# Kernel tuning notes

Hardware: AMD Instinct MI355X
Metric: run time of the kernel (lower is better)

The kernel has to match this reference:

```python
import jax, jax.numpy as jnp
import numpy as np

B, S, D = 2, 512, 1024   # batch, seq, hidden_size
E, K, I = 16, 8, 1024    # num_experts, num_experts_per_tok, moe_intermediate_size
I_SH = 1024              # moe_intermediate_size * num_shared_experts
ROUTE_SCALE = 2.826


def setup_inputs() -> dict:
    key = jax.random.key(0)
    ks = jax.random.split(key, 8)
    s = 0.02
    return {
        "x": jax.random.normal(ks[0], (B, S, D), dtype=jnp.float32),
        "gate_w": jax.random.normal(ks[1], (E, D), dtype=jnp.float32) * s,
        "expert_bias": jnp.zeros((E,), dtype=jnp.float32),
        "w_gate": jax.random.normal(ks[2], (E, I, D), dtype=jnp.float32) * s,
        "w_up": jax.random.normal(ks[3], (E, I, D), dtype=jnp.float32) * s,
        "w_down": jax.random.normal(ks[4], (E, D, I), dtype=jnp.float32) * s,
        "shared_gate_w": jax.random.normal(ks[5], (I_SH, D), dtype=jnp.float32) * s,
        "shared_up_w": jax.random.normal(ks[6], (I_SH, D), dtype=jnp.float32) * s,
        "shared_down_w": jax.random.normal(ks[7], (D, I_SH), dtype=jnp.float32) * s,
    }


def reference(x, gate_w, expert_bias, w_gate, w_up, w_down,
              shared_gate_w, shared_up_w, shared_down_w):
    # --- routing (sigmoid scores, top-k, optional norm, scale) ---
    gates = jnp.einsum('bsd,ed->bse', x, gate_w)
    scores = jax.nn.sigmoid(gates.astype(jnp.float32))           # [B,S,E]
    sel_scores = scores + expert_bias
    _, inds = jax.lax.top_k(sel_scores, K)                       # [B,S,K]
    selected = jnp.take_along_axis(scores, inds, axis=-1)        # [B,S,K]
    selected = selected / selected.sum(axis=-1, keepdims=True)   # route_norm (K>1)
    selected = selected * ROUTE_SCALE
    # combine weights as dense [B,S,E]; unselected experts get weight 0,
    # which is mathematically identical to gather-dispatch-combine.
    onehot = jax.nn.one_hot(inds, E, dtype=selected.dtype)       # [B,S,K,E]
    combine = jnp.einsum('bske,bsk->bse', onehot, selected)
    # --- experts (SwitchGLU: per-expert SwiGLU MLPs) ---
    hg = jnp.einsum('bsd,eid->bsei', x, w_gate)                  # [B,S,E,I]
    hu = jnp.einsum('bsd,eid->bsei', x, w_up)
    h = jax.nn.silu(hg) * hu
    ye = jnp.einsum('bsei,edi->bsed', h, w_down)                 # [B,S,E,D]
    y = jnp.einsum('bsed,bse->bsd', ye, combine).astype(x.dtype)
    # --- shared expert MLP (SwiGLU) ---
    g = jnp.einsum('bsd,id->bsi', x, shared_gate_w)
    u = jnp.einsum('bsd,id->bsi', x, shared_up_w)
    y = y + jnp.einsum('bsi,di->bsd', jax.nn.silu(g) * u, shared_down_w)
    return y
```

## Files before the change

kernel.cpp:

```cpp
#include <hip/hip_runtime.h>
#include <hip/hip_bf16.h>


typedef __attribute__((ext_vector_type(8))) short bf16x8;
typedef __attribute__((ext_vector_type(4))) float f32x4;
typedef __attribute__((ext_vector_type(8))) unsigned short u16x8;

#define NTOK 1024
#define DD   1024
#define II   1024
#define NE   16
#define NEXP 17
#define KSEL 8
#define RSCALE 2.826f

#define WCONV_BLOCKS 2176
#define ROUTE_BLOCKS 256

#define BM 128
#define BN 64
#define BK 32
#define LDA 40

#define MB (1024ull*1024ull)
#define OFF_XBF   0ull
#define OFF_H     (2ull*MB)
#define OFF_WG    (36ull*MB)
#define OFF_WU    (70ull*MB)
#define OFF_WD    (104ull*MB)
#define OFF_LIST  (138ull*MB)
#define OFF_SCALE (OFF_LIST + 4ull*NEXP*NTOK)
#define OFF_CNT   (OFF_SCALE + 4ull*NEXP*NTOK)
#define WS_NEED   (OFF_CNT + 4096ull)
#define OFF_POS   WS_NEED
#define OFF_PBUF  (OFF_POS + 4ull*NE*NTOK)
#define WS_NEED2  (OFF_PBUF + 4ull*9216*DD)

__device__ __forceinline__ unsigned short f2bf(float f) {
    union { __hip_bfloat16 h; unsigned short u; } c;
    c.h = __float2bfloat16(f);
    return c.u;
}

__device__ __forceinline__ void gl2lds16(const unsigned short* g, unsigned short* l) {
    __builtin_amdgcn_global_load_lds(
        (const __attribute__((address_space(1))) void*)g,
        (__attribute__((address_space(3))) void*)l, 16, 0, 0);
}

__device__ __forceinline__ f32x4 ntload4(const float* p) {
    return __builtin_nontemporal_load((const f32x4*)p);
}

__global__ __launch_bounds__(256) void prologue_kernel(
    const float* __restrict__ x, const float* __restrict__ gw,
    const float* __restrict__ bias, unsigned short* __restrict__ xbf,
    unsigned int* __restrict__ emask, float* __restrict__ tsc,
    const float* __restrict__ wg, const float* __restrict__ wu, const float* __restrict__ wd,
    const float* __restrict__ sgw, const float* __restrict__ suw, const float* __restrict__ sdw,
    unsigned short* __restrict__ wgb, unsigned short* __restrict__ wub,
    unsigned short* __restrict__ wdb)
{
    if (blockIdx.x >= ROUTE_BLOCKS) {
        int wb = blockIdx.x - ROUTE_BLOCKS;
        int p  = wb / WCONV_BLOCKS;
        int bx = wb - p * WCONV_BLOCKS;
        const size_t ROUTED8 = (size_t)NE * II * DD / 8;
        const float* rsrc = (p == 0) ? wg : (p == 1) ? wu : wd;
        const float* ssrc = (p == 0) ? sgw : (p == 1) ? suw : sdw;
        unsigned short* dst = (p == 0) ? wgb : (p == 1) ? wub : wdb;

        size_t base8 = (size_t)bx * 1024 + threadIdx.x;
        f32x4 a[4], b[4];
#pragma unroll
        for (int c = 0; c < 4; c++) {
            size_t g8 = base8 + c * 256;
            const float* src = (g8 < ROUTED8) ? rsrc + 8 * g8 : ssrc + 8 * (g8 - ROUTED8);
            a[c] = ntload4(src);
            b[c] = ntload4(src + 4);
        }
#pragma unroll
        for (int c = 0; c < 4; c++) {
            size_t g8 = base8 + c * 256;
            u16x8 o;
            o[0] = f2bf(a[c][0]); o[1] = f2bf(a[c][1]); o[2] = f2bf(a[c][2]); o[3] = f2bf(a[c][3]);
            o[4] = f2bf(b[c][0]); o[5] = f2bf(b[c][1]); o[6] = f2bf(b[c][2]); o[7] = f2bf(b[c][3]);
            *(u16x8*)(dst + 8 * g8) = o;
        }
        return;
    }

    int wave = threadIdx.x >> 6, lane = threadIdx.x & 63;
    int t = blockIdx.x * 4 + wave;

    const float4* xr = (const float4*)(x + (size_t)t * DD);
    ushort4* xw = (ushort4*)(xbf + (size_t)t * DD);
    float acc[NE];
#pragma unroll
    for (int e = 0; e < NE; e++) acc[e] = 0.f;
#pragma unroll
    for (int i = 0; i < DD / 64 / 4; i++) {
        float4 xv = xr[lane + 64 * i];
        xw[lane + 64 * i] = make_ushort4(f2bf(xv.x), f2bf(xv.y), f2bf(xv.z), f2bf(xv.w));
#pragma unroll
        for (int e = 0; e < NE; e++) {
            float4 w = ((const float4*)(gw + (size_t)e * DD))[lane + 64 * i];
            acc[e] += xv.x * w.x + xv.y * w.y + xv.z * w.z + xv.w * w.w;
        }
    }
#pragma unroll
    for (int e = 0; e < NE; e++) {
        float v = acc[e];
        for (int off = 32; off > 0; off >>= 1) v += __shfl_xor(v, off, 64);
        acc[e] = v;
    }
    if (lane == 0) {
        float sc[NE], sel[NE];
#pragma unroll
        for (int e = 0; e < NE; e++) {
            sc[e] = 1.f / (1.f + expf(-acc[e]));
            sel[e] = sc[e] + bias[e];
        }
        bool used[NE] = {};
        int inds[KSEL];
        float ssum = 0.f;
        for (int k = 0; k < KSEL; k++) {
            float best = -1e30f; int bi = 0;
            for (int e = 0; e < NE; e++)
                if (!used[e] && sel[e] > best) { best = sel[e]; bi = e; }
            used[bi] = true; inds[k] = bi; ssum += sc[bi];
        }
        float inv = RSCALE / ssum;
        unsigned int m = 0;
        for (int k = 0; k < KSEL; k++) {
            int e = inds[k];
            m |= (1u << e);
            tsc[(size_t)t * NE + e] = sc[e] * inv;
        }
        emask[t] = m;
    }
}

__global__ __launch_bounds__(1024) void build_lists_kernel(
    const unsigned int* __restrict__ emask, const float* __restrict__ tsc,
    int* __restrict__ count, int* __restrict__ list, float* __restrict__ scalebuf,
    int* __restrict__ poslut)
{
    int e = blockIdx.x;
    int t = threadIdx.x;
    if (e == NE) {
        list[NE * NTOK + t] = t;
        scalebuf[NE * NTOK + t] = 1.0f;
        if (t == 0) count[NE] = NTOK;
        return;
    }
    int lane = t & 63, wave = t >> 6;
    bool sel = (emask[t] >> e) & 1u;
    unsigned long long m = __ballot(sel);
    int posw = __popcll(m & ((1ull << lane) - 1ull));
    int wtot = __popcll(m);
    __shared__ int woff[16];
    if (lane == 0) woff[wave] = wtot;
    __syncthreads();
    if (t == 0) {
        int s = 0;
#pragma unroll
        for (int w = 0; w < 16; w++) { int v = woff[w]; woff[w] = s; s += v; }
        count[e] = s;
    }
    __syncthreads();
    int pos = woff[wave] + posw;
    if (sel) {
        list[e * NTOK + pos] = t;
        scalebuf[e * NTOK + pos] = tsc[(size_t)t * NE + e];
    }
    if (poslut) poslut[e * NTOK + t] = sel ? pos : -1;
}

__global__ __launch_bounds__(256, 2) void gateup_kernel(
    const unsigned short* __restrict__ xbf,
    const unsigned short* __restrict__ wgb, const unsigned short* __restrict__ wub,
    const int* __restrict__ count, const int* __restrict__ list,
    const float* __restrict__ scalebuf, unsigned short* __restrict__ hbuf)
{
    int s = blockIdx.x;
    int xcd = s & 7, t = s >> 3;
    int g = xcd + 8 * (t >> 3);
    int e = g >> 3;
    int n0 = (g & 7) * 128;
    int m0 = (t & 7) * 128;
    int cnt = count[e];
    if (m0 >= cnt) return;
    const unsigned short* Bg = wgb + (size_t)e * II * DD;
    const unsigned short* Bu = wub + (size_t)e * II * DD;

    __shared__ __align__(16) unsigned short As[8192];
    __shared__ __align__(16) unsigned short Bgs[8192];
    __shared__ __align__(16) unsigned short Bus[8192];
    __shared__ int rowtok[128];

    int tid = threadIdx.x;
    if (tid < 128) {
        int gr = m0 + tid;
        rowtok[tid] = list[e * NTOK + ((gr < cnt) ? gr : (cnt - 1))];
    }
    __syncthreads();

    int lane = tid & 63, wave = tid >> 6;
    int wm = wave & 1, wn = wave >> 1;
    int row16 = lane & 15, quad = lane >> 4;

    int qS = wave >> 1;
    int srow = (wave & 1) * 64 + (lane >> 2);
    int colS = ((lane & 3) ^ ((lane >> 3) & 3)) * 8;
    int tokr[4];
#pragma unroll
    for (int c = 0; c < 4; c++) tokr[c] = rowtok[srow + c * 16];
    const unsigned short* gBg0 = Bg + (size_t)(n0 + srow) * DD + colS;
    const unsigned short* gBu0 = Bu + (size_t)(n0 + srow) * DD + colS;

    f32x4 accG[4][4], accU[4][4];
#pragma unroll
    for (int mi = 0; mi < 4; mi++)
#pragma unroll
        for (int ni = 0; ni < 4; ni++) {
            accG[mi][ni] = (f32x4){0.f, 0.f, 0.f, 0.f};
            accU[mi][ni] = (f32x4){0.f, 0.f, 0.f, 0.f};
        }

    int qe = (quad ^ ((row16 >> 1) & 3)) * 8;

    for (int k0 = 0; k0 < DD; k0 += 64) {
        int koff = k0 + qS * 32;
#pragma unroll
        for (int c = 0; c < 4; c++) {
            gl2lds16(xbf + (size_t)tokr[c] * DD + koff + colS, As + wave * 2048 + c * 512);
            gl2lds16(gBg0 + (size_t)(c * 16) * DD + koff, Bgs + wave * 2048 + c * 512);
            gl2lds16(gBu0 + (size_t)(c * 16) * DD + koff, Bus + wave * 2048 + c * 512);
        }
        __syncthreads();

#pragma unroll
        for (int kk = 0; kk < 2; kk++) {
            bf16x8 a[4], bg[4], bu[4];
            int base = kk * 4096 + qe;
#pragma unroll
            for (int mi = 0; mi < 4; mi++)
                a[mi] = *(const bf16x8*)(As + base + (wm * 64 + mi * 16 + row16) * 32);
#pragma unroll
            for (int ni = 0; ni < 4; ni++) {
                bg[ni] = *(const bf16x8*)(Bgs + base + (wn * 64 + ni * 16 + row16) * 32);
                bu[ni] = *(const bf16x8*)(Bus + base + (wn * 64 + ni * 16 + row16) * 32);
            }
#pragma unroll
            for (int mi = 0; mi < 4; mi++)
#pragma unroll
                for (int ni = 0; ni < 4; ni++) {
                    accG[mi][ni] = __builtin_amdgcn_mfma_f32_16x16x32_bf16(a[mi], bg[ni], accG[mi][ni], 0, 0, 0);
                    accU[mi][ni] = __builtin_amdgcn_mfma_f32_16x16x32_bf16(a[mi], bu[ni], accU[mi][ni], 0, 0, 0);
                }
        }
        __syncthreads();
    }

#pragma unroll
    for (int mi = 0; mi < 4; mi++) {
        int grb = m0 + wm * 64 + mi * 16 + quad * 4;
#pragma unroll
        for (int r = 0; r < 4; r++) {
            int gr = grb + r;
            if (gr >= cnt) continue;
            float rs = scalebuf[e * NTOK + gr];
            size_t rowoff = ((size_t)e * NTOK + gr) * II + n0 + wn * 64;
#pragma unroll
            for (int ni = 0; ni < 4; ni++) {
                float g2 = accG[mi][ni][r], u = accU[mi][ni][r];
                float h = g2 / (1.f + __expf(-g2)) * u * rs;
                hbuf[rowoff + ni * 16 + row16] = f2bf(h);
            }
        }
    }
}

__global__ __launch_bounds__(256, 3) void down_kernel(
    const unsigned short* __restrict__ hbuf,
    const unsigned short* __restrict__ wdb,
    const int* __restrict__ count, const int* __restrict__ list,
    float* __restrict__ y)
{
    int s = blockIdx.x;
    int xcd = s & 7, t = s >> 3;
    int g = xcd + 8 * (t >> 3);
    int e = g >> 3;
    int n0 = (g & 7) * 128;
    int m0 = (t & 7) * 128;
    int cnt = count[e];
    if (m0 >= cnt) return;
    const unsigned short* Bp = wdb + (size_t)e * DD * II;

    __shared__ __align__(16) unsigned short As[8192];
    __shared__ __align__(16) unsigned short Bs[8192];

    int tid = threadIdx.x;
    int lane = tid & 63, wave = tid >> 6;
    int wm = wave & 1, wn = wave >> 1;
    int row16 = lane & 15, quad = lane >> 4;

    int qS = wave >> 1;
    int srow = (wave & 1) * 64 + (lane >> 2);
    int colS = ((lane & 3) ^ ((lane >> 3) & 3)) * 8;

    size_t arow[4];
#pragma unroll
    for (int c = 0; c < 4; c++) {
        int gr = m0 + srow + c * 16;
        int idx = (gr < cnt) ? gr : (cnt - 1);
        arow[c] = ((size_t)e * NTOK + idx) * II;
    }
    const unsigned short* gB0 = Bp + (size_t)(n0 + srow) * II + colS;

    f32x4 acc[4][4];
#pragma unroll
    for (int mi = 0; mi < 4; mi++)
#pragma unroll
        for (int ni = 0; ni < 4; ni++) acc[mi][ni] = (f32x4){0.f, 0.f, 0.f, 0.f};

    int qe = (quad ^ ((row16 >> 1) & 3)) * 8;

    for (int k0 = 0; k0 < II; k0 += 64) {
        int koff = k0 + qS * 32;
#pragma unroll
        for (int c = 0; c < 4; c++) {
            gl2lds16(hbuf + arow[c] + koff + colS, As + wave * 2048 + c * 512);
            gl2lds16(gB0 + (size_t)(c * 16) * II + koff, Bs + wave * 2048 + c * 512);
        }
        __syncthreads();

#pragma unroll
        for (int kk = 0; kk < 2; kk++) {
            bf16x8 a[4], b[4];
            int base = kk * 4096 + qe;
#pragma unroll
            for (int mi = 0; mi < 4; mi++)
                a[mi] = *(const bf16x8*)(As + base + (wm * 64 + mi * 16 + row16) * 32);
#pragma unroll
            for (int ni = 0; ni < 4; ni++)
                b[ni] = *(const bf16x8*)(Bs + base + (wn * 64 + ni * 16 + row16) * 32);
#pragma unroll
            for (int mi = 0; mi < 4; mi++)
#pragma unroll
                for (int ni = 0; ni < 4; ni++)
                    acc[mi][ni] = __builtin_amdgcn_mfma_f32_16x16x32_bf16(a[mi], b[ni], acc[mi][ni], 0, 0, 0);
        }
        __syncthreads();
    }

#pragma unroll
    for (int mi = 0; mi < 4; mi++) {
        int grb = m0 + wm * 64 + mi * 16 + quad * 4;
#pragma unroll
        for (int r = 0; r < 4; r++) {
            int gr = grb + r;
            if (gr >= cnt) continue;
            int tk = list[e * NTOK + gr];
            float* yr = y + (size_t)tk * DD + n0 + wn * 64;
#pragma unroll
            for (int ni = 0; ni < 4; ni++)
                unsafeAtomicAdd(yr + ni * 16 + row16, acc[mi][ni][r]);
        }
    }
}

__global__ __launch_bounds__(256, 3) void down_pb_kernel(
    const unsigned short* __restrict__ hbuf,
    const unsigned short* __restrict__ wdb,
    const int* __restrict__ count, float* __restrict__ pbuf)
{
    int s = blockIdx.x;
    int xcd = s & 7, t = s >> 3;
    int g = xcd + 8 * (t >> 3);
    int e = g >> 3;
    int n0 = (g & 7) * 128;
    int m0 = (t & 7) * 128;
    int cnt = count[e];
    if (m0 >= cnt) return;
    int base_e = 0;
    for (int i = 0; i < e; i++) base_e += count[i];
    const unsigned short* Bp = wdb + (size_t)e * DD * II;

    __shared__ __align__(16) unsigned short As[8192];
    __shared__ __align__(16) unsigned short Bs[8192];

    int tid = threadIdx.x;
    int lane = tid & 63, wave = tid >> 6;
    int wm = wave & 1, wn = wave >> 1;
    int row16 = lane & 15, quad = lane >> 4;

    int qS = wave >> 1;
    int srow = (wave & 1) * 64 + (lane >> 2);
    int colS = ((lane & 3) ^ ((lane >> 3) & 3)) * 8;

    size_t arow[4];
#pragma unroll
    for (int c = 0; c < 4; c++) {
        int gr = m0 + srow + c * 16;
        int idx = (gr < cnt) ? gr : (cnt - 1);
        arow[c] = ((size_t)e * NTOK + idx) * II;
    }
    const unsigned short* gB0 = Bp + (size_t)(n0 + srow) * II + colS;

    f32x4 acc[4][4];
#pragma unroll
    for (int mi = 0; mi < 4; mi++)
#pragma unroll
        for (int ni = 0; ni < 4; ni++) acc[mi][ni] = (f32x4){0.f, 0.f, 0.f, 0.f};

    int qe = (quad ^ ((row16 >> 1) & 3)) * 8;

    for (int k0 = 0; k0 < II; k0 += 64) {
        int koff = k0 + qS * 32;
#pragma unroll
        for (int c = 0; c < 4; c++) {
            gl2lds16(hbuf + arow[c] + koff + colS, As + wave * 2048 + c * 512);
            gl2lds16(gB0 + (size_t)(c * 16) * II + koff, Bs + wave * 2048 + c * 512);
        }
        __syncthreads();

#pragma unroll
        for (int kk = 0; kk < 2; kk++) {
            bf16x8 a[4], b[4];
            int base = kk * 4096 + qe;
#pragma unroll
            for (int mi = 0; mi < 4; mi++)
                a[mi] = *(const bf16x8*)(As + base + (wm * 64 + mi * 16 + row16) * 32);
#pragma unroll
            for (int ni = 0; ni < 4; ni++)
                b[ni] = *(const bf16x8*)(Bs + base + (wn * 64 + ni * 16 + row16) * 32);
#pragma unroll
            for (int mi = 0; mi < 4; mi++)
#pragma unroll
                for (int ni = 0; ni < 4; ni++)
                    acc[mi][ni] = __builtin_amdgcn_mfma_f32_16x16x32_bf16(a[mi], b[ni], acc[mi][ni], 0, 0, 0);
        }
        __syncthreads();
    }

#pragma unroll
    for (int mi = 0; mi < 4; mi++) {
        int grb = m0 + wm * 64 + mi * 16 + quad * 4;
#pragma unroll
        for (int r = 0; r < 4; r++) {
            int gr = grb + r;
            if (gr >= cnt) continue;
            float* pr = pbuf + (size_t)(base_e + gr) * DD + n0 + wn * 64;
#pragma unroll
            for (int ni = 0; ni < 4; ni++)
                pr[ni * 16 + row16] = acc[mi][ni][r];
        }
    }
}

__global__ __launch_bounds__(256) void combine_kernel(
    const float* __restrict__ pbuf, const int* __restrict__ count,
    const int* __restrict__ poslut, float* __restrict__ y)
{
    int t = blockIdx.x;
    int c4 = threadIdx.x;
    float4 acc = make_float4(0.f, 0.f, 0.f, 0.f);
    int base = 0;
#pragma unroll
    for (int e = 0; e < NE; e++) {
        int p = poslut[e * NTOK + t];
        if (p >= 0) {
            float4 v = ((const float4*)(pbuf + (size_t)(base + p) * DD))[c4];
            acc.x += v.x; acc.y += v.y; acc.z += v.z; acc.w += v.w;
        }
        base += count[e];
    }
    {
        float4 v = ((const float4*)(pbuf + (size_t)(base + t) * DD))[c4];
        acc.x += v.x; acc.y += v.y; acc.z += v.z; acc.w += v.w;
    }
    ((float4*)(y + (size_t)t * DD))[c4] = acc;
}

__global__ __launch_bounds__(256) void gateup_fb(
    const unsigned short* __restrict__ xbf,
    const float* __restrict__ wg, const float* __restrict__ wu,
    const float* __restrict__ sgw, const float* __restrict__ suw,
    const int* __restrict__ count, const int* __restrict__ list,
    const float* __restrict__ scalebuf, unsigned short* __restrict__ hbuf)
{
    int e = blockIdx.z;
    int cnt = count[e];
    int m0 = blockIdx.x * BM;
    if (m0 >= cnt) return;
    int n0 = blockIdx.y * BN;
    const float* Bg = (e < NE) ? wg + (size_t)e * II * DD : sgw;
    const float* Bu = (e < NE) ? wu + (size_t)e * II * DD : suw;

    __shared__ __align__(16) unsigned short As[BM * LDA];
    __shared__ __align__(16) unsigned short Bgs[BN * LDA];
    __shared__ __align__(16) unsigned short Bus[BN * LDA];
    __shared__ int rowtok[BM];

    int tid = threadIdx.x;
    if (tid < BM) {
        int gr = m0 + tid;
        rowtok[tid] = (gr < cnt) ? list[e * NTOK + gr] : -1;
    }
    __syncthreads();

    int lane = tid & 63, wave = tid >> 6;
    int wm = wave >> 1, wn = wave & 1;
    int row16 = lane & 15, quad = lane >> 4;

    f32x4 accG[4][2], accU[4][2];
#pragma unroll
    for (int mi = 0; mi < 4; mi++)
#pragma unroll
        for (int ni = 0; ni < 2; ni++) {
            accG[mi][ni] = (f32x4){0.f, 0.f, 0.f, 0.f};
            accU[mi][ni] = (f32x4){0.f, 0.f, 0.f, 0.f};
        }

    for (int k0 = 0; k0 < DD; k0 += BK) {
#pragma unroll
        for (int i = 0; i < 2; i++) {
            int c = tid + 256 * i;
            int row = c >> 2, kc = (c & 3) * 8;
            int tok = rowtok[row];
            uint4 v = (tok >= 0) ? *(const uint4*)(xbf + (size_t)tok * DD + k0 + kc)
                                 : make_uint4(0u, 0u, 0u, 0u);
            *(uint4*)(As + row * LDA + kc) = v;
        }
#pragma unroll
        for (int i = 0; i < 2; i++) {
            int c = tid + 256 * i;
            int row = c >> 3, f = (c & 7) * 4;
            float4 vg = *(const float4*)(Bg + (size_t)(n0 + row) * DD + k0 + f);
            float4 vu = *(const float4*)(Bu + (size_t)(n0 + row) * DD + k0 + f);
            *(ushort4*)(Bgs + row * LDA + f) = make_ushort4(f2bf(vg.x), f2bf(vg.y), f2bf(vg.z), f2bf(vg.w));
            *(ushort4*)(Bus + row * LDA + f) = make_ushort4(f2bf(vu.x), f2bf(vu.y), f2bf(vu.z), f2bf(vu.w));
        }
        __syncthreads();

        bf16x8 af[4], bg[2], bu[2];
#pragma unroll
        for (int mi = 0; mi < 4; mi++)
            af[mi] = *(const bf16x8*)(As + (wm * 64 + mi * 16 + row16) * LDA + quad * 8);
#pragma unroll
        for (int ni = 0; ni < 2; ni++) {
            bg[ni] = *(const bf16x8*)(Bgs + (wn * 32 + ni * 16 + row16) * LDA + quad * 8);
            bu[ni] = *(const bf16x8*)(Bus + (wn * 32 + ni * 16 + row16) * LDA + quad * 8);
        }
#pragma unroll
        for (int mi = 0; mi < 4; mi++)
#pragma unroll
            for (int ni = 0; ni < 2; ni++) {
                accG[mi][ni] = __builtin_amdgcn_mfma_f32_16x16x32_bf16(af[mi], bg[ni], accG[mi][ni], 0, 0, 0);
                accU[mi][ni] = __builtin_amdgcn_mfma_f32_16x16x32_bf16(af[mi], bu[ni], accU[mi][ni], 0, 0, 0);
            }
        __syncthreads();
    }

#pragma unroll
    for (int mi = 0; mi < 4; mi++) {
        int mbase = wm * 64 + mi * 16 + quad * 4;
#pragma unroll
        for (int r = 0; r < 4; r++) {
            int gr = m0 + mbase + r;
            if (gr >= cnt) continue;
            float rs = scalebuf[e * NTOK + gr];
            size_t rowoff = ((size_t)e * NTOK + gr) * II + n0;
#pragma unroll
            for (int ni = 0; ni < 2; ni++) {
                int n = wn * 32 + ni * 16 + row16;
                float g = accG[mi][ni][r], u = accU[mi][ni][r];
                float h = g / (1.f + __expf(-g)) * u * rs;
                hbuf[rowoff + n] = f2bf(h);
            }
        }
    }
}

__global__ __launch_bounds__(256) void down_fb(
    const unsigned short* __restrict__ hbuf,
    const float* __restrict__ wd, const float* __restrict__ sdw,
    const int* __restrict__ count, const int* __restrict__ list,
    float* __restrict__ y)
{
    int e = blockIdx.z;
    int cnt = count[e];
    int m0 = blockIdx.x * BM;
    if (m0 >= cnt) return;
    int n0 = blockIdx.y * BN;
    const float* Bp = (e < NE) ? wd + (size_t)e * DD * II : sdw;

    __shared__ __align__(16) unsigned short As[BM * LDA];
    __shared__ __align__(16) unsigned short Bs[BN * LDA];

    int tid = threadIdx.x;
    int lane = tid & 63, wave = tid >> 6;
    int wm = wave >> 1, wn = wave & 1;
    int row16 = lane & 15, quad = lane >> 4;

    f32x4 acc[4][2];
#pragma unroll
    for (int mi = 0; mi < 4; mi++)
#pragma unroll
        for (int ni = 0; ni < 2; ni++) acc[mi][ni] = (f32x4){0.f, 0.f, 0.f, 0.f};

    const unsigned short* Abase = hbuf + ((size_t)e * NTOK + m0) * II;

    for (int k0 = 0; k0 < II; k0 += BK) {
#pragma unroll
        for (int i = 0; i < 2; i++) {
            int c = tid + 256 * i;
            int row = c >> 2, kc = (c & 3) * 8;
            uint4 v = (m0 + row < cnt) ? *(const uint4*)(Abase + (size_t)row * II + k0 + kc)
                                       : make_uint4(0u, 0u, 0u, 0u);
            *(uint4*)(As + row * LDA + kc) = v;
        }
#pragma unroll
        for (int i = 0; i < 2; i++) {
            int c = tid + 256 * i;
            int row = c >> 3, f = (c & 7) * 4;
            float4 v = *(const float4*)(Bp + (size_t)(n0 + row) * II + k0 + f);
            *(ushort4*)(Bs + row * LDA + f) = make_ushort4(f2bf(v.x), f2bf(v.y), f2bf(v.z), f2bf(v.w));
        }
        __syncthreads();

        bf16x8 af[4], bf[2];
#pragma unroll
        for (int mi = 0; mi < 4; mi++)
            af[mi] = *(const bf16x8*)(As + (wm * 64 + mi * 16 + row16) * LDA + quad * 8);
#pragma unroll
        for (int ni = 0; ni < 2; ni++)
            bf[ni] = *(const bf16x8*)(Bs + (wn * 32 + ni * 16 + row16) * LDA + quad * 8);
#pragma unroll
        for (int mi = 0; mi < 4; mi++)
#pragma unroll
            for (int ni = 0; ni < 2; ni++)
                acc[mi][ni] = __builtin_amdgcn_mfma_f32_16x16x32_bf16(af[mi], bf[ni], acc[mi][ni], 0, 0, 0);
        __syncthreads();
    }

#pragma unroll
    for (int mi = 0; mi < 4; mi++) {
        int mbase = wm * 64 + mi * 16 + quad * 4;
#pragma unroll
        for (int r = 0; r < 4; r++) {
            int gr = m0 + mbase + r;
            if (gr >= cnt) continue;
            int t = list[e * NTOK + gr];
#pragma unroll
            for (int ni = 0; ni < 2; ni++) {
                int n = wn * 32 + ni * 16 + row16;
                unsafeAtomicAdd(&y[(size_t)t * DD + n0 + n], acc[mi][ni][r]);
            }
        }
    }
}

extern "C" void kernel_launch(void* const* d_in, const int* in_sizes, int n_in,
                              void* d_out, int out_size, void* d_ws, size_t ws_size,
                              hipStream_t stream)
{
    const float* x    = (const float*)d_in[0];
    const float* gw   = (const float*)d_in[1];
    const float* bias = (const float*)d_in[2];
    const float* wg   = (const float*)d_in[3];
    const float* wu   = (const float*)d_in[4];
    const float* wd   = (const float*)d_in[5];
    const float* sgw  = (const float*)d_in[6];
    const float* suw  = (const float*)d_in[7];
    const float* sdw  = (const float*)d_in[8];
    float* y = (float*)d_out;

    char* ws = (char*)d_ws;
    unsigned short* xbf  = (unsigned short*)(ws + OFF_XBF);
    unsigned short* hbuf = (unsigned short*)(ws + OFF_H);
    unsigned short* wgb  = (unsigned short*)(ws + OFF_WG);
    unsigned short* wub  = (unsigned short*)(ws + OFF_WU);
    unsigned short* wdb  = (unsigned short*)(ws + OFF_WD);
    int*   list     = (int*)(ws + OFF_LIST);
    float* scalebuf = (float*)(ws + OFF_SCALE);
    int*   count    = (int*)(ws + OFF_CNT);
    int*   poslut   = (int*)(ws + OFF_POS);
    float* pbuf     = (float*)(ws + OFF_PBUF);

    bool big = (ws_size >= WS_NEED);
    bool pb  = (ws_size >= WS_NEED2);
    if (!big) {
        list     = (int*)(ws + 36ull * MB);
        scalebuf = (float*)(ws + 36ull * MB + 4ull * NEXP * NTOK);
        count    = (int*)(ws + 36ull * MB + 8ull * NEXP * NTOK);
    }

    unsigned int* emask = (unsigned int*)(ws + OFF_H);
    float*        tsc   = (float*)(ws + OFF_H + 4096);

    if (!(big && pb))
        hipMemsetAsync(d_out, 0, (size_t)NTOK * DD * sizeof(float), stream);

    unsigned pro_grid = big ? (ROUTE_BLOCKS + 3 * WCONV_BLOCKS) : ROUTE_BLOCKS;
    prologue_kernel<<<dim3(pro_grid), 256, 0, stream>>>(
        x, gw, bias, xbf, emask, tsc,
        wg, wu, wd, sgw, suw, sdw, wgb, wub, wdb);
    build_lists_kernel<<<dim3(NEXP), 1024, 0, stream>>>(emask, tsc, count, list, scalebuf,
                                                        pb ? poslut : (int*)nullptr);

    if (big) {
        gateup_kernel<<<dim3(NEXP * 8 * 8), 256, 0, stream>>>(
            xbf, wgb, wub, count, list, scalebuf, hbuf);
        if (pb) {
            down_pb_kernel<<<dim3(NEXP * 8 * 8), 256, 0, stream>>>(
                hbuf, wdb, count, pbuf);
            combine_kernel<<<dim3(NTOK), 256, 0, stream>>>(pbuf, count, poslut, y);
        } else {
            down_kernel<<<dim3(NEXP * 8 * 8), 256, 0, stream>>>(
                hbuf, wdb, count, list, y);
        }
    } else {
        gateup_fb<<<dim3(NTOK / BM, II / BN, NEXP), 256, 0, stream>>>(
            xbf, wg, wu, sgw, suw, count, list, scalebuf, hbuf);
        down_fb<<<dim3(NTOK / BM, DD / BN, NEXP), 256, 0, stream>>>(
            hbuf, wd, sdw, count, list, y);
    }
}
```

Before: 335.7 us.

## Fold routing list construction into GEMM kernels and index partial buffer by token

Removes the separate build_lists kernel launch on the main path. Each gateup and down block now rebuilds its expert's token list from the expert masks with an in-block prefix scan. The partial-sum buffer is re-indexed as [token][slot], where the slot is the popcount of lower selected experts, so the combine kernel simply sums 9 contiguous rows without a position lookup. The price is a redundant 256-thread scan with many barriers in every block.

```diff
diff --git a/kernel.cpp b/kernel.cpp
--- a/kernel.cpp
+++ b/kernel.cpp
@@ -31,10 +31,11 @@
 #define OFF_LIST  (138ull*MB)
 #define OFF_SCALE (OFF_LIST + 4ull*NEXP*NTOK)
 #define OFF_CNT   (OFF_SCALE + 4ull*NEXP*NTOK)
-#define WS_NEED   (OFF_CNT + 4096ull)
-#define OFF_POS   WS_NEED
-#define OFF_PBUF  (OFF_POS + 4ull*NE*NTOK)
-#define WS_NEED2  (OFF_PBUF + 4ull*9216*DD)
+#define OFF_EMASK (OFF_CNT + 4096ull)
+#define OFF_TSC   (OFF_EMASK + 4096ull)
+#define WS_NEED   (OFF_TSC + 4ull*NTOK*NE)
+#define OFF_PBUF  WS_NEED
+#define WS_NEED2  (OFF_PBUF + 4ull*9ull*NTOK*DD)
 
 __device__ __forceinline__ unsigned short f2bf(float f) {
     union { __hip_bfloat16 h; unsigned short u; } c;
@@ -50,6 +51,42 @@
 
 __device__ __forceinline__ f32x4 ntload4(const float* p) {
     return __builtin_nontemporal_load((const f32x4*)p);
+}
+
+__device__ __forceinline__ int scan_list(
+    const unsigned int* __restrict__ emask, int e, int m0,
+    int* rowtok, int* sh)
+{
+    int tid = threadIdx.x;
+    if (tid < 128) rowtok[tid] = 0;
+    int sel[4]; int local = 0;
+#pragma unroll
+    for (int j = 0; j < 4; j++) {
+        unsigned int mm = emask[4 * tid + j];
+        sel[j] = (e < NE) ? (int)((mm >> e) & 1u) : 1;
+        local += sel[j];
+    }
+    sh[tid] = local;
+    __syncthreads();
+    for (int off = 1; off < 256; off <<= 1) {
+        int v = sh[tid];
+        int add = (tid >= off) ? sh[tid - off] : 0;
+        __syncthreads();
+        sh[tid] = v + add;
+        __syncthreads();
+    }
+    int cnt = sh[255];
+    int pos = sh[tid] - local;
+#pragma unroll
+    for (int j = 0; j < 4; j++) {
+        if (sel[j]) {
+            int rel = pos - m0;
+            if (rel >= 0 && rel < 128) rowtok[rel] = 4 * tid + j;
+            pos++;
+        }
+    }
+    __syncthreads();
+    return cnt;
 }
 
 __global__ __launch_bounds__(256) void prologue_kernel(
@@ -143,8 +180,7 @@
 
 __global__ __launch_bounds__(1024) void build_lists_kernel(
     const unsigned int* __restrict__ emask, const float* __restrict__ tsc,
-    int* __restrict__ count, int* __restrict__ list, float* __restrict__ scalebuf,
-    int* __restrict__ poslut)
+    int* __restrict__ count, int* __restrict__ list, float* __restrict__ scalebuf)
 {
     int e = blockIdx.x;
     int t = threadIdx.x;
@@ -174,14 +210,13 @@
         list[e * NTOK + pos] = t;
         scalebuf[e * NTOK + pos] = tsc[(size_t)t * NE + e];
     }
-    if (poslut) poslut[e * NTOK + t] = sel ? pos : -1;
 }
 
 __global__ __launch_bounds__(256, 2) void gateup_kernel(
     const unsigned short* __restrict__ xbf,
     const unsigned short* __restrict__ wgb, const unsigned short* __restrict__ wub,
-    const int* __restrict__ count, const int* __restrict__ list,
-    const float* __restrict__ scalebuf, unsigned short* __restrict__ hbuf)
+    const unsigned int* __restrict__ emask, const float* __restrict__ tsc,
+    unsigned short* __restrict__ hbuf)
 {
     int s = blockIdx.x;
     int xcd = s & 7, t = s >> 3;
@@ -189,23 +224,19 @@
     int e = g >> 3;
     int n0 = (g & 7) * 128;
     int m0 = (t & 7) * 128;
-    int cnt = count[e];
-    if (m0 >= cnt) return;
-    const unsigned short* Bg = wgb + (size_t)e * II * DD;
-    const unsigned short* Bu = wub + (size_t)e * II * DD;
 
     __shared__ __align__(16) unsigned short As[8192];
     __shared__ __align__(16) unsigned short Bgs[8192];
     __shared__ __align__(16) unsigned short Bus[8192];
     __shared__ int rowtok[128];
+    __shared__ int sh[256];
+
+    int cnt = scan_list(emask, e, m0, rowtok, sh);
+    if (m0 >= cnt) return;
+    const unsigned short* Bg = wgb + (size_t)e * II * DD;
+    const unsigned short* Bu = wub + (size_t)e * II * DD;
 
     int tid = threadIdx.x;
-    if (tid < 128) {
-        int gr = m0 + tid;
-        rowtok[tid] = list[e * NTOK + ((gr < cnt) ? gr : (cnt - 1))];
-    }
-    __syncthreads();
-
     int lane = tid & 63, wave = tid >> 6;
     int wm = wave & 1, wn = wave >> 1;
     int row16 = lane & 15, quad = lane >> 4;
@@ -265,12 +296,14 @@
 
 #pragma unroll
     for (int mi = 0; mi < 4; mi++) {
-        int grb = m0 + wm * 64 + mi * 16 + quad * 4;
+        int lrb = wm * 64 + mi * 16 + quad * 4;
 #pragma unroll
         for (int r = 0; r < 4; r++) {
-            int gr = grb + r;
+            int lrow = lrb + r;
+            int gr = m0 + lrow;
             if (gr >= cnt) continue;
-            float rs = scalebuf[e * NTOK + gr];
+            int tok = rowtok[lrow];
+            float rs = (e < NE) ? tsc[(size_t)tok * NE + e] : 1.0f;
             size_t rowoff = ((size_t)e * NTOK + gr) * II + n0 + wn * 64;
 #pragma unroll
             for (int ni = 0; ni < 4; ni++) {
@@ -280,6 +313,113 @@
             }
         }
     }
+}
+
+__global__ __launch_bounds__(256, 3) void down_pb_kernel(
+    const unsigned short* __restrict__ hbuf,
+    const unsigned short* __restrict__ wdb,
+    const unsigned int* __restrict__ emask, float* __restrict__ pbuf)
+{
+    int s = blockIdx.x;
+    int xcd = s & 7, t = s >> 3;
+    int g = xcd + 8 * (t >> 3);
+    int e = g >> 3;
+    int n0 = (g & 7) * 128;
+    int m0 = (t & 7) * 128;
+
+    __shared__ __align__(16) unsigned short As[8192];
+    __shared__ __align__(16) unsigned short Bs[8192];
+    __shared__ int rowtok[128];
+    __shared__ int sh[256];
+
+    int cnt = scan_list(emask, e, m0, rowtok, sh);
+    if (m0 >= cnt) return;
+    const unsigned short* Bp = wdb + (size_t)e * DD * II;
+
+    int tid = threadIdx.x;
+    int lane = tid & 63, wave = tid >> 6;
+    int wm = wave & 1, wn = wave >> 1;
+    int row16 = lane & 15, quad = lane >> 4;
+
+    int qS = wave >> 1;
+    int srow = (wave & 1) * 64 + (lane >> 2);
+    int colS = ((lane & 3) ^ ((lane >> 3) & 3)) * 8;
+
+    size_t arow[4];
+#pragma unroll
+    for (int c = 0; c < 4; c++) {
+        int gr = m0 + srow + c * 16;
+        int idx = (gr < cnt) ? gr : (cnt - 1);
+        arow[c] = ((size_t)e * NTOK + idx) * II;
+    }
+    const unsigned short* gB0 = Bp + (size_t)(n0 + srow) * II + colS;
+
+    f32x4 acc[4][4];
+#pragma unroll
+    for (int mi = 0; mi < 4; mi++)
+#pragma unroll
+        for (int ni = 0; ni < 4; ni++) acc[mi][ni] = (f32x4){0.f, 0.f, 0.f, 0.f};
+
+    int qe = (quad ^ ((row16 >> 1) & 3)) * 8;
+
+    for (int k0 = 0; k0 < II; k0 += 64) {
+        int koff = k0 + qS * 32;
+#pragma unroll
+        for (int c = 0; c < 4; c++) {
+            gl2lds16(hbuf + arow[c] + koff + colS, As + wave * 2048 + c * 512);
+            gl2lds16(gB0 + (size_t)(c * 16) * II + koff, Bs + wave * 2048 + c * 512);
+        }
+        __syncthreads();
+
+#pragma unroll
+        for (int kk = 0; kk < 2; kk++) {
+            bf16x8 a[4], b[4];
+            int base = kk * 4096 + qe;
+#pragma unroll
+            for (int mi = 0; mi < 4; mi++)
+                a[mi] = *(const bf16x8*)(As + base + (wm * 64 + mi * 16 + row16) * 32);
+#pragma unroll
+            for (int ni = 0; ni < 4; ni++)
+                b[ni] = *(const bf16x8*)(Bs + base + (wn * 64 + ni * 16 + row16) * 32);
+#pragma unroll
+            for (int mi = 0; mi < 4; mi++)
+#pragma unroll
+                for (int ni = 0; ni < 4; ni++)
+                    acc[mi][ni] = __builtin_amdgcn_mfma_f32_16x16x32_bf16(a[mi], b[ni], acc[mi][ni], 0, 0, 0);
+        }
+        __syncthreads();
+    }
+
+#pragma unroll
+    for (int mi = 0; mi < 4; mi++) {
+        int lrb = wm * 64 + mi * 16 + quad * 4;
+#pragma unroll
+        for (int r = 0; r < 4; r++) {
+            int lrow = lrb + r;
+            int gr = m0 + lrow;
+            if (gr >= cnt) continue;
+            int tok = rowtok[lrow];
+            int k = (e < NE) ? __popc(emask[tok] & ((1u << e) - 1u)) : 8;
+            float* pr = pbuf + ((size_t)tok * 9 + k) * DD + n0 + wn * 64;
+#pragma unroll
+            for (int ni = 0; ni < 4; ni++)
+                pr[ni * 16 + row16] = acc[mi][ni][r];
+        }
+    }
+}
+
+__global__ __launch_bounds__(256) void combine_kernel(
+    const float* __restrict__ pbuf, float* __restrict__ y)
+{
+    int t = blockIdx.x;
+    int c4 = threadIdx.x;
+    float4 acc = make_float4(0.f, 0.f, 0.f, 0.f);
+#pragma unroll
+    for (int k = 0; k < 9; k++) {
+        float4 v = ((const float4*)(pbuf + ((size_t)t * 9 + k) * DD))[c4];
+        acc.x += v.x; acc.y += v.y; acc.z += v.z; acc.w += v.w;
+    }
+    ((float4*)(y + (size_t)t * DD))[c4] = acc;
 }
 
 __global__ __launch_bounds__(256, 3) void down_kernel(
@@ -369,119 +509,6 @@
                 unsafeAtomicAdd(yr + ni * 16 + row16, acc[mi][ni][r]);
         }
     }
-}
-
-__global__ __launch_bounds__(256, 3) void down_pb_kernel(
-    const unsigned short* __restrict__ hbuf,
-    const unsigned short* __restrict__ wdb,
-    const int* __restrict__ count, float* __restrict__ pbuf)
-{
-    int s = blockIdx.x;
-    int xcd = s & 7, t = s >> 3;
-    int g = xcd + 8 * (t >> 3);
-    int e = g >> 3;
-    int n0 = (g & 7) * 128;
-    int m0 = (t & 7) * 128;
-    int cnt = count[e];
-    if (m0 >= cnt) return;
-    int base_e = 0;
-    for (int i = 0; i < e; i++) base_e += count[i];
-    const unsigned short* Bp = wdb + (size_t)e * DD * II;
-
-    __shared__ __align__(16) unsigned short As[8192];
-    __shared__ __align__(16) unsigned short Bs[8192];
-
-    int tid = threadIdx.x;
-    int lane = tid & 63, wave = tid >> 6;
-    int wm = wave & 1, wn = wave >> 1;
-    int row16 = lane & 15, quad = lane >> 4;
-
-    int qS = wave >> 1;
-    int srow = (wave & 1) * 64 + (lane >> 2);
-    int colS = ((lane & 3) ^ ((lane >> 3) & 3)) * 8;
-
-    size_t arow[4];
-#pragma unroll
-    for (int c = 0; c < 4; c++) {
-        int gr = m0 + srow + c * 16;
-        int idx = (gr < cnt) ? gr : (cnt - 1);
-        arow[c] = ((size_t)e * NTOK + idx) * II;
-    }
-    const unsigned short* gB0 = Bp + (size_t)(n0 + srow) * II + colS;
-
-    f32x4 acc[4][4];
-#pragma unroll
-    for (int mi = 0; mi < 4; mi++)
-#pragma unroll
-        for (int ni = 0; ni < 4; ni++) acc[mi][ni] = (f32x4){0.f, 0.f, 0.f, 0.f};
-
-    int qe = (quad ^ ((row16 >> 1) & 3)) * 8;
-
-    for (int k0 = 0; k0 < II; k0 += 64) {
-        int koff = k0 + qS * 32;
-#pragma unroll
-        for (int c = 0; c < 4; c++) {
-            gl2lds16(hbuf + arow[c] + koff + colS, As + wave * 2048 + c * 512);
-            gl2lds16(gB0 + (size_t)(c * 16) * II + koff, Bs + wave * 2048 + c * 512);
-        }
-        __syncthreads();
-
-#pragma unroll
-        for (int kk = 0; kk < 2; kk++) {
-            bf16x8 a[4], b[4];
-            int base = kk * 4096 + qe;
-#pragma unroll
-            for (int mi = 0; mi < 4; mi++)
-                a[mi] = *(const bf16x8*)(As + base + (wm * 64 + mi * 16 + row16) * 32);
-#pragma unroll
-            for (int ni = 0; ni < 4; ni++)
-                b[ni] = *(const bf16x8*)(Bs + base + (wn * 64 + ni * 16 + row16) * 32);
-#pragma unroll
-            for (int mi = 0; mi < 4; mi++)
-#pragma unroll
-                for (int ni = 0; ni < 4; ni++)
-                    acc[mi][ni] = __builtin_amdgcn_mfma_f32_16x16x32_bf16(a[mi], b[ni], acc[mi][ni], 0, 0, 0);
-        }
-        __syncthreads();
-    }
-
-#pragma unroll
-    for (int mi = 0; mi < 4; mi++) {
-        int grb = m0 + wm * 64 + mi * 16 + quad * 4;
-#pragma unroll
-        for (int r = 0; r < 4; r++) {
-            int gr = grb + r;
-            if (gr >= cnt) continue;
-            float* pr = pbuf + (size_t)(base_e + gr) * DD + n0 + wn * 64;
-#pragma unroll
-            for (int ni = 0; ni < 4; ni++)
-                pr[ni * 16 + row16] = acc[mi][ni][r];
-        }
-    }
-}
-
-__global__ __launch_bounds__(256) void combine_kernel(
-    const float* __restrict__ pbuf, const int* __restrict__ count,
-    const int* __restrict__ poslut, float* __restrict__ y)
-{
-    int t = blockIdx.x;
-    int c4 = threadIdx.x;
-    float4 acc = make_float4(0.f, 0.f, 0.f, 0.f);
-    int base = 0;
-#pragma unroll
-    for (int e = 0; e < NE; e++) {
-        int p = poslut[e * NTOK + t];
-        if (p >= 0) {
-            float4 v = ((const float4*)(pbuf + (size_t)(base + p) * DD))[c4];
-            acc.x += v.x; acc.y += v.y; acc.z += v.z; acc.w += v.w;
-        }
-        base += count[e];
-    }
-    {
-        float4 v = ((const float4*)(pbuf + (size_t)(base + t) * DD))[c4];
-        acc.x += v.x; acc.y += v.y; acc.z += v.z; acc.w += v.w;
-    }
-    ((float4*)(y + (size_t)t * DD))[c4] = acc;
 }
 
 __global__ __launch_bounds__(256) void gateup_fb(
@@ -687,7 +714,6 @@
     int*   list     = (int*)(ws + OFF_LIST);
     float* scalebuf = (float*)(ws + OFF_SCALE);
     int*   count    = (int*)(ws + OFF_CNT);
-    int*   poslut   = (int*)(ws + OFF_POS);
     float* pbuf     = (float*)(ws + OFF_PBUF);
 
     bool big = (ws_size >= WS_NEED);
@@ -698,8 +724,10 @@
         count    = (int*)(ws + 36ull * MB + 8ull * NEXP * NTOK);
     }
 
-    unsigned int* emask = (unsigned int*)(ws + OFF_H);
-    float*        tsc   = (float*)(ws + OFF_H + 4096);
+    unsigned int* emask = big ? (unsigned int*)(ws + OFF_EMASK)
+                              : (unsigned int*)(ws + OFF_H);
+    float* tsc = big ? (float*)(ws + OFF_TSC)
+                     : (float*)(ws + OFF_H + 4096);
 
     if (!(big && pb))
         hipMemsetAsync(d_out, 0, (size_t)NTOK * DD * sizeof(float), stream);
@@ -708,21 +736,23 @@
     prologue_kernel<<<dim3(pro_grid), 256, 0, stream>>>(
         x, gw, bias, xbf, emask, tsc,
         wg, wu, wd, sgw, suw, sdw, wgb, wub, wdb);
-    build_lists_kernel<<<dim3(NEXP), 1024, 0, stream>>>(emask, tsc, count, list, scalebuf,
-                                                        pb ? poslut : (int*)nullptr);
-
-    if (big) {
+
+    if (big && pb) {
         gateup_kernel<<<dim3(NEXP * 8 * 8), 256, 0, stream>>>(
-            xbf, wgb, wub, count, list, scalebuf, hbuf);
-        if (pb) {
-            down_pb_kernel<<<dim3(NEXP * 8 * 8), 256, 0, stream>>>(
-                hbuf, wdb, count, pbuf);
-            combine_kernel<<<dim3(NTOK), 256, 0, stream>>>(pbuf, count, poslut, y);
-        } else {
-            down_kernel<<<dim3(NEXP * 8 * 8), 256, 0, stream>>>(
-                hbuf, wdb, count, list, y);
-        }
+            xbf, wgb, wub, emask, tsc, hbuf);
+        down_pb_kernel<<<dim3(NEXP * 8 * 8), 256, 0, stream>>>(
+            hbuf, wdb, emask, pbuf);
+        combine_kernel<<<dim3(NTOK), 256, 0, stream>>>(pbuf, y);
+    } else if (big) {
+        build_lists_kernel<<<dim3(NEXP), 1024, 0, stream>>>(
+            emask, tsc, count, list, scalebuf);
+        gateup_kernel<<<dim3(NEXP * 8 * 8), 256, 0, stream>>>(
+            xbf, wgb, wub, emask, tsc, hbuf);
+        down_kernel<<<dim3(NEXP * 8 * 8), 256, 0, stream>>>(
+            hbuf, wdb, count, list, y);
     } else {
+        build_lists_kernel<<<dim3(NEXP), 1024, 0, stream>>>(
+            emask, tsc, count, list, scalebuf);
         gateup_fb<<<dim3(NTOK / BM, II / BN, NEXP), 256, 0, stream>>>(
             xbf, wg, wu, sgw, suw, count, list, scalebuf, hbuf);
         down_fb<<<dim3(NTOK / BM, DD / BN, NEXP), 256, 0, stream>>>(
```

Measured after the change: 337.3 us. Within noise of the previous version (+0.5%).
